# Performance work log

Measured on AMD Instinct MI355X. Metric: run time of the kernel, lower is better.

## Reference

```python
import jax, jax.numpy as jnp
import numpy as np
from jax import lax


def _kaiming_uniform(key, shape):
    fan_in = shape[1]
    bound = np.sqrt(6.0 / fan_in)
    return jax.random.uniform(key, shape, jnp.float32, -bound, bound)


def rbf_conv(x, w, k, pad):
    # x: [B,C,H,W]; w: [O, C*k*k]. Equivalent to F.unfold + torch.cdist (p=2).
    patches = lax.conv_general_dilated_patches(
        x, (k, k), (1, 1), [(pad, pad), (pad, pad)])  # [B, C*k*k, Ho, Wo]
    B, D, Ho, Wo = patches.shape
    p = patches.reshape(B, D, Ho * Wo)                 # [B, D, L]
    pn = jnp.sum(p * p, axis=1)                        # [B, L]
    wn = jnp.sum(w * w, axis=1)                        # [O]
    cross = jnp.einsum('bdl,od->bol', p, w)            # [B, O, L]
    d2 = pn[:, None, :] + wn[None, :, None] - 2.0 * cross
    d = jnp.sqrt(jnp.maximum(d2, 0.0))
    return d.reshape(B, w.shape[0], Ho, Wo)


def sfm(x, alpha):
    # non-overlapping (fh,fw) blocks, elementwise alpha weight, mean-pool
    B, C, H, W = x.shape
    fh, fw = alpha.shape
    xb = x.reshape(B, C, H // fh, fh, W // fw, fw).transpose(0, 1, 2, 4, 3, 5)
    return jnp.mean(xb * alpha, axis=(-2, -1))         # [B,C,H//fh,W//fw]


def gauss_act(d, std):
    return jnp.exp(d * d / (-2.0 * std * std))


def crelu(x, bias):
    return x * (x >= bias).astype(x.dtype)


def basic_block(x, w, std, bias, alpha, k, pad):
    d = rbf_conv(x, w, k, pad)
    return sfm(crelu(gauss_act(d, std), bias), alpha)


def setup_inputs() -> dict:
    key = jax.random.key(0)
    ks = jax.random.split(key, 8)
    x = jax.random.normal(ks[0], (16, 3, 128, 128), jnp.float32)
    w1 = _kaiming_uniform(ks[1], (96, 3 * 5 * 5))
    w2 = _kaiming_uniform(ks[2], (192, 96 * 5 * 5))
    w3 = _kaiming_uniform(ks[3], (384, 192 * 3 * 3))
    alpha = jnp.linspace(0.9, 0.99, 4, dtype=jnp.float32).reshape(2, 2)
    fc_w = jax.random.normal(ks[4], (100, 384 * 32 * 32), jnp.float32) * 0.01
    fc_b = jnp.zeros((100,), jnp.float32)
    return {
        'x': x,
        'w1': w1, 'std1': jnp.array([2.0], jnp.float32), 'bias1': jnp.array([0.3], jnp.float32), 'alpha1': alpha,
        'w2': w2, 'std2': jnp.array([2.0], jnp.float32), 'bias2': jnp.array([0.3], jnp.float32), 'alpha2': alpha,
        'w3': w3, 'std3': jnp.array([2.0], jnp.float32), 'bias3': jnp.array([0.3], jnp.float32),
        'fc_w': fc_w, 'fc_b': fc_b,
    }


def reference(x, w1, std1, bias1, alpha1, w2, std2, bias2, alpha2,
              w3, std3, bias3, fc_w, fc_b):
    h = basic_block(x, w1, std1, bias1, alpha1, 5, 2)      # [16,96,64,64]
    h = basic_block(h, w2, std2, bias2, alpha2, 5, 2)      # [16,192,32,32]
    d = rbf_conv(h, w3, 3, 1)                              # [16,384,32,32]
    h = crelu(gauss_act(d, std3), bias3)
    out = h.reshape(x.shape[0], -1) @ fc_w.T + fc_b        # [16,100]
    return out
```

## Files before the change

### kernel.cpp

```cpp
#include <hip/hip_runtime.h>

#define TPB 256

typedef short bf16x8 __attribute__((ext_vector_type(8)));
typedef float f32x4 __attribute__((ext_vector_type(4)));

__device__ inline unsigned short f2bf(float f) {
    unsigned int u = __float_as_uint(f);
    unsigned int r = (u + 0x7fffu + ((u >> 16) & 1u)) >> 16;
    return (unsigned short)r;
}
__device__ inline float bf2f(unsigned short h) {
    return __uint_as_float(((unsigned int)h) << 16);
}

__device__ __forceinline__ void gl16(void* lds, const void* g) {
    __builtin_amdgcn_global_load_lds(
        (const __attribute__((address_space(1))) unsigned int*)g,
        (__attribute__((address_space(3))) unsigned int*)lds, 16, 0, 0);
}

__global__ void prep_all(const float* __restrict__ x,
                         const float* __restrict__ w1, const float* __restrict__ w2,
                         const float* __restrict__ w3,
                         unsigned short* __restrict__ xbf,
                         unsigned short* __restrict__ w1r, unsigned short* __restrict__ w2r,
                         unsigned short* __restrict__ w3r, unsigned short* __restrict__ zerob,
                         float* __restrict__ wn1, float* __restrict__ wn2,
                         float* __restrict__ wn3) {
    int bid = blockIdx.x;
    int tid = threadIdx.x;
    if (bid < 1024) {
        int idx = bid * TPB + tid;
        int b = idx >> 14, px = idx & 16383;
        const float* xb = x + (size_t)b * 3 * 16384 + px;
        float v0 = xb[0], v1 = xb[16384], v2 = xb[32768];
        ushort4 v;
        v.x = f2bf(v0); v.y = f2bf(v1); v.z = f2bf(v2);
        v.w = f2bf(v0 * v0 + v1 * v1 + v2 * v2);
        *(ushort4*)&xbf[(size_t)idx * 4] = v;
    } else if (bid < 4388) {
        int idx = (bid - 1024) * TPB + tid;
        if (idx < 13056) {
            int o = idx / 136, d = idx - o * 136;
            int tp = d >> 2, c = d & 3;
            float v = 0.f;
            if (tp < 30) {
                int ki = tp / 6, kj = tp - 6 * ki;
                if (kj < 5) v = (c < 3) ? w1[o * 75 + c * 25 + ki * 5 + kj] : -0.5f;
            }
            w1r[idx] = f2bf(v);
        } else if (idx < 492288) {
            int i = idx - 13056;
            int c = i & 31; int r = i >> 5;
            int o = r % 192; r /= 192;
            int tap = r % 26; int cg = r / 26;
            float v = 0.f;
            if (tap < 25) v = w2[((size_t)o * 96 + cg * 32 + c) * 25 + tap];
            w2r[i] = f2bf(v);
        } else if (idx < 860928) {
            int i = idx - 492288;
            int c = i & 31; int r = i >> 5;
            int o = r % 192; r /= 192;
            int tap = r % 10; int cg = r / 10;
            float v = 0.f;
            if (tap < 9) v = w3[((size_t)o * 192 + cg * 32 + c) * 9 + tap];
            w3r[i] = f2bf(v);
        } else if (idx < 860992) {
            zerob[idx - 860928] = 0;
        }
    } else {
        int o = (bid - 4388) * 4 + (tid >> 6);
        int lane = tid & 63;
        const float* row; float* dst; int D;
        if (o < 96)       { row = w1 + (size_t)o * 75;           D = 75;   dst = wn1 + o; }
        else if (o < 288) { int r = o - 96;  row = w2 + (size_t)r * 2400; D = 2400; dst = wn2 + r; }
        else              { int r = o - 288; row = w3 + (size_t)r * 1728; D = 1728; dst = wn3 + r; }
        float acc = 0.f;
        for (int i = lane; i < D; i += 64) { float v = row[i]; acc += v * v; }
        #pragma unroll
        for (int off = 32; off >= 1; off >>= 1) acc += __shfl_down(acc, off);
        if (lane == 0) *dst = acc;
    }
}

__launch_bounds__(256, 2)
__global__ void conv1_mfma(const unsigned short* __restrict__ xbf,
                           const unsigned short* __restrict__ w1r,
                           const float* __restrict__ wn,
                           const float* __restrict__ stdp, const float* __restrict__ biasp,
                           const float* __restrict__ alphap,
                           unsigned short* __restrict__ out,
                           float* __restrict__ sqout)
{
    __shared__ unsigned short in_s[22 * 20 * 4];
    __shared__ unsigned short w_s[96 * 136];

    int bid = blockIdx.x;
    int tx = bid & 7; bid >>= 3;
    int ty = bid & 7; bid >>= 3;
    int b = bid;
    int x0 = tx * 16, y0 = ty * 16;
    int tid = threadIdx.x;
    int lane = tid & 63, wv = tid >> 6;
    int col = lane & 15, kg = lane >> 4;

    for (int idx = tid; idx < 21 * 20; idx += 256) {
        int py = idx / 20, px = idx - py * 20;
        int gy = y0 - 2 + py, gx = x0 - 2 + px;
        ushort4 v = make_ushort4(0, 0, 0, 0);
        if (gy >= 0 && gy < 128 && gx >= 0 && gx < 128)
            v = *(const ushort4*)&xbf[(((size_t)b * 128 + gy) * 128 + gx) * 4];
        *(ushort4*)&in_s[idx * 4] = v;
    }
    for (int idx = tid; idx < 1632; idx += 256)
        *(bf16x8*)&w_s[idx * 8] = *(const bf16x8*)&w1r[idx * 8];
    __syncthreads();

    f32x4 acc[6][4];
    #pragma unroll
    for (int mt = 0; mt < 6; ++mt)
        #pragma unroll
        for (int n = 0; n < 4; ++n) acc[mt][n] = (f32x4){0.f, 0.f, 0.f, 0.f};

    #pragma unroll
    for (int ks = 0; ks < 4; ++ks) {
        int tap0 = ks * 8 + kg * 2;
        int ki = tap0 / 6, kj = tap0 - 6 * ki;
        bf16x8 bfrag[4];
        #pragma unroll
        for (int n = 0; n < 4; ++n) {
            int row = wv * 4 + n + ki;
            int ix = col + kj;
            const unsigned short* p = &in_s[(row * 20 + ix) * 4];
            union { bf16x8 v; uint2 u[2]; } tmp;
            tmp.u[0] = *(const uint2*)p;
            tmp.u[1] = *(const uint2*)(p + 4);
            bfrag[n] = tmp.v;
        }
        bf16x8 afrag[6];
        #pragma unroll
        for (int mt = 0; mt < 6; ++mt)
            afrag[mt] = *(const bf16x8*)&w_s[(mt * 16 + col) * 136 + ks * 32 + kg * 8];
        #pragma unroll
        for (int mt = 0; mt < 6; ++mt)
            #pragma unroll
            for (int n = 0; n < 4; ++n)
                acc[mt][n] = __builtin_amdgcn_mfma_f32_16x16x32_bf16(
                    afrag[mt], bfrag[n], acc[mt][n], 0, 0, 0);
    }

    float stdv = stdp[0], biasv = biasp[0];
    float inv2s2 = 1.f / (2.f * stdv * stdv);
    float a00 = alphap[0], a01 = alphap[1], a10 = alphap[2], a11 = alphap[3];
    int dx = col & 1;
    float ax0 = dx ? a01 : a00;
    float ax1 = dx ? a11 : a10;

    float sqa[2] = {0.f, 0.f};
    #pragma unroll
    for (int mt = 0; mt < 6; ++mt) {
        #pragma unroll
        for (int p2 = 0; p2 < 2; ++p2) {
            unsigned short res[4];
            #pragma unroll
            for (int r = 0; r < 4; ++r) {
                int o = mt * 16 + kg * 4 + r;
                float wno = wn[o];
                float d20 = fmaxf(wno - 2.f * acc[mt][2 * p2][r], 0.f);
                float d21 = fmaxf(wno - 2.f * acc[mt][2 * p2 + 1][r], 0.f);
                float g0 = __expf(-d20 * inv2s2);
                float g1 = __expf(-d21 * inv2s2);
                g0 = (g0 >= biasv) ? g0 : 0.f;
                g1 = (g1 >= biasv) ? g1 : 0.f;
                float s = ax0 * g0 + ax1 * g1;
                s += __shfl_xor(s, 1);
                res[r] = f2bf(0.25f * s);
                float vv = bf2f(res[r]);
                sqa[p2] += vv * vv;
            }
            if (dx == 0) {
                int yo = ty * 8 + wv * 2 + p2, xo = tx * 8 + (col >> 1);
                *(ushort4*)&out[(((size_t)b * 64 + yo) * 64 + xo) * 96 + mt * 16 + kg * 4] =
                    make_ushort4(res[0], res[1], res[2], res[3]);
            }
        }
    }
    #pragma unroll
    for (int p2 = 0; p2 < 2; ++p2) {
        float s = sqa[p2];
        s += __shfl_xor(s, 16);
        s += __shfl_xor(s, 32);
        if (dx == 0 && kg == 0) {
            int yo = ty * 8 + wv * 2 + p2, xo = tx * 8 + (col >> 1);
            sqout[((size_t)b * 64 + yo) * 64 + xo] = s;
        }
    }
}

__launch_bounds__(128, 2)
__global__ void conv2_mfma(const unsigned short* __restrict__ hin,
                           const unsigned short* __restrict__ wt2,
                           const float* __restrict__ sq1,
                           const float* __restrict__ wn,
                           const float* __restrict__ stdp, const float* __restrict__ biasp,
                           const float* __restrict__ alphap,
                           const unsigned short* __restrict__ zerob,
                           unsigned short* __restrict__ hout)
{
    __shared__ unsigned short in_s[240 * 32];
    __shared__ unsigned short w_s[2][2 * 96 * 32];
    __shared__ float sq_s[12 * 20];
    __shared__ int s_nz[2];

    int bid = blockIdx.x;
    int xt = bid & 3; bid >>= 2;
    int yt = bid & 7; bid >>= 3;
    int ot = bid & 1; int b = bid >> 1;
    int x0 = xt * 16, y0 = yt * 8, o0 = ot * 96;
    int tid = threadIdx.x;
    int lane = tid & 63, wave_n = tid >> 6;
    int col = lane & 15, kg = lane >> 4;

    #pragma unroll
    for (int i = 0; i < 2; ++i) {
        int sidx = tid + i * 128;
        if (sidx < 240) {
            int r = sidx / 20, c = sidx - r * 20;
            int gy = y0 - 2 + r, gx = x0 - 2 + c;
            float v = 0.f;
            if (gy >= 0 && gy < 64 && gx >= 0 && gx < 64)
                v = sq1[((size_t)b * 64 + gy) * 64 + gx];
            sq_s[sidx] = v;
        }
    }

    f32x4 acc[6][4];
    #pragma unroll
    for (int mt = 0; mt < 6; ++mt)
        #pragma unroll
        for (int nt = 0; nt < 4; ++nt) acc[mt][nt] = (f32x4){0.f, 0.f, 0.f, 0.f};

    for (int cg = 0; cg < 3; ++cg) {
        #pragma unroll
        for (int i = 0; i < 8; ++i) {
            int chunk = tid + i * 128;
            if (chunk < 960) {
                int px = chunk >> 2, c16 = chunk & 3;
                int iy = px / 20, ix = px - iy * 20;
                int gy = y0 - 2 + iy, gx = x0 - 2 + ix;
                const void* src = (gy >= 0 && gy < 64 && gx >= 0 && gx < 64)
                    ? (const void*)&hin[(((size_t)b * 64 + gy) * 64 + gx) * 96 + cg * 32 + c16 * 8]
                    : (const void*)zerob;
                gl16(&in_s[chunk * 8], src);
            }
        }
        #pragma unroll
        for (int i = 0; i < 6; ++i) {
            int chunk = tid + i * 128;
            int tp = chunk / 384, rem = chunk - tp * 384;
            gl16(&w_s[0][tp * 3072 + rem * 8],
                 &wt2[(((size_t)cg * 26 + tp) * 192 + o0) * 32 + rem * 8]);
        }
        __syncthreads();

        unsigned int nzb = 0;
        #pragma unroll
        for (int i = 0; i < 8; ++i) {
            int chunk = tid + i * 128;
            if (chunk < 960) {
                uint4 v = *(const uint4*)&in_s[chunk * 8];
                nzb |= v.x | v.y | v.z | v.w;
            }
        }
        bool any = __any(nzb != 0);
        if (lane == 0) s_nz[wave_n] = any ? 1 : 0;
        __syncthreads();
        if (s_nz[0] | s_nz[1]) {
            for (int pr = 0; pr < 13; ++pr) {
                int cur = pr & 1;
                if (pr < 12) {
                    #pragma unroll
                    for (int i = 0; i < 6; ++i) {
                        int chunk = tid + i * 128;
                        int tp = chunk / 384, rem = chunk - tp * 384;
                        gl16(&w_s[cur ^ 1][tp * 3072 + rem * 8],
                             &wt2[(((size_t)cg * 26 + (pr + 1) * 2 + tp) * 192 + o0) * 32 + rem * 8]);
                    }
                }
                #pragma unroll
                for (int t2 = 0; t2 < 2; ++t2) {
                    int tap = pr * 2 + t2;
                    int ki = tap / 5, kj = tap - 5 * ki;
                    if (tap >= 25) { ki = 0; kj = 0; }
                    bf16x8 bfrag[4], afrag[6];
                    #pragma unroll
                    for (int nt = 0; nt < 4; ++nt) {
                        int yy = 2 * nt + (col >> 3) + ki;
                        int xx = wave_n * 8 + (col & 7) + kj;
                        bfrag[nt] = *(const bf16x8*)&in_s[(yy * 20 + xx) * 32 + kg * 8];
                    }
                    #pragma unroll
                    for (int mt = 0; mt < 6; ++mt)
                        afrag[mt] = *(const bf16x8*)
                            &w_s[cur][(t2 * 96 + mt * 16 + col) * 32 + kg * 8];
                    #pragma unroll
                    for (int mt = 0; mt < 6; ++mt)
                        #pragma unroll
                        for (int nt = 0; nt < 4; ++nt)
                            acc[mt][nt] = __builtin_amdgcn_mfma_f32_16x16x32_bf16(
                                afrag[mt], bfrag[nt], acc[mt][nt], 0, 0, 0);
                }
                __syncthreads();
            }
        }
    }

    float stdv = stdp[0], biasv = biasp[0];
    float inv2s2 = 1.f / (2.f * stdv * stdv);
    float a_own = alphap[(col >> 3) * 2 + (col & 1)];
    #pragma unroll
    for (int nt = 0; nt < 4; ++nt) {
        int ly = 2 * nt + (col >> 3) + 2;
        int lx = wave_n * 8 + (col & 7) + 2;
        float pnv = 0.f;
        #pragma unroll
        for (int dy = -2; dy <= 2; ++dy)
            #pragma unroll
            for (int dx2 = -2; dx2 <= 2; ++dx2)
                pnv += sq_s[(ly + dy) * 20 + (lx + dx2)];
        int y = y0 + 2 * nt + (col >> 3);
        int x = x0 + wave_n * 8 + (col & 7);
        int yo = (y0 >> 1) + nt;
        int xo = x >> 1;
        #pragma unroll
        for (int mt = 0; mt < 6; ++mt) {
            int ob = o0 + mt * 16 + (kg << 2);
            unsigned short res[4];
            #pragma unroll
            for (int r = 0; r < 4; ++r) {
                float d2 = fmaxf(pnv + wn[ob + r] - 2.f * acc[mt][nt][r], 0.f);
                float g = __expf(-d2 * inv2s2);
                g = (g >= biasv) ? g : 0.f;
                g *= a_own;
                g += __shfl_xor(g, 1);
                g += __shfl_xor(g, 8);
                res[r] = f2bf(0.25f * g);
            }
            if (((col & 1) == 0) && ((col & 8) == 0)) {
                *(ushort4*)&hout[(((size_t)b * 32 + yo) * 32 + xo) * 192 + ob] =
                    make_ushort4(res[0], res[1], res[2], res[3]);
            }
        }
        (void)y;
    }
}

__launch_bounds__(256, 1)
__global__ void conv3_mfma(const unsigned short* __restrict__ hin,
                           const unsigned short* __restrict__ wt3,
                           const float* __restrict__ wn,
                           const float* __restrict__ stdp, const float* __restrict__ biasp,
                           const unsigned short* __restrict__ zerob,
                           unsigned short* __restrict__ hout)
{
    __shared__ unsigned short in_s[324 * 32];
    __shared__ unsigned short w_s[2][2 * 96 * 32];
    __shared__ float pnacc[324];

    int bid = blockIdx.x;
    int sp = bid & 3; bid >>= 2;
    int ot = bid & 3; int b = bid >> 2;
    int x0 = (sp & 1) * 16, y0 = (sp >> 1) * 16, o0 = ot * 96;
    int tid = threadIdx.x;
    int lane = tid & 63, wvn = tid >> 6;
    int col = lane & 15, kg = lane >> 4;

    for (int i = tid; i < 324; i += 256) pnacc[i] = 0.f;

    f32x4 acc[6][4];
    #pragma unroll
    for (int mt = 0; mt < 6; ++mt)
        #pragma unroll
        for (int nt = 0; nt < 4; ++nt) acc[mt][nt] = (f32x4){0.f, 0.f, 0.f, 0.f};

    for (int cg = 0; cg < 6; ++cg) {
        #pragma unroll
        for (int i = 0; i < 6; ++i) {
            int chunk = tid + i * 256;
            if (chunk < 1296) {
                int px = chunk >> 2, c16 = chunk & 3;
                int iy = px / 18, ix = px - iy * 18;
                int gy = y0 - 1 + iy, gx = x0 - 1 + ix;
                const void* src = (gy >= 0 && gy < 32 && gx >= 0 && gx < 32)
                    ? (const void*)&hin[(((size_t)b * 32 + gy) * 32 + gx) * 192 + cg * 32 + c16 * 8]
                    : (const void*)zerob;
                gl16(&in_s[chunk * 8], src);
            }
        }
        #pragma unroll
        for (int i = 0; i < 3; ++i) {
            int chunk = tid + i * 256;
            int tp = chunk / 384, rem = chunk - tp * 384;
            gl16(&w_s[0][tp * 3072 + rem * 8],
                 &wt3[(((size_t)cg * 10 + tp) * 192 + o0) * 32 + rem * 8]);
        }
        __syncthreads();

        #pragma unroll
        for (int i = 0; i < 2; ++i) {
            int px = tid + i * 256;
            if (px < 324) {
                const unsigned short* p = &in_s[px * 32];
                float a = 0.f;
                #pragma unroll
                for (int c = 0; c < 32; c += 8) {
                    bf16x8 v = *(const bf16x8*)&p[c];
                    #pragma unroll
                    for (int j = 0; j < 8; ++j) { float f = bf2f((unsigned short)v[j]); a += f * f; }
                }
                pnacc[px] += a;
            }
        }

        for (int pr = 0; pr < 5; ++pr) {
            int cur = pr & 1;
            if (pr < 4) {
                #pragma unroll
                for (int i = 0; i < 3; ++i) {
                    int chunk = tid + i * 256;
                    int tp = chunk / 384, rem = chunk - tp * 384;
                    gl16(&w_s[cur ^ 1][tp * 3072 + rem * 8],
                         &wt3[(((size_t)cg * 10 + (pr + 1) * 2 + tp) * 192 + o0) * 32 + rem * 8]);
                }
            }
            #pragma unroll
            for (int t2 = 0; t2 < 2; ++t2) {
                int tap = pr * 2 + t2;
                int ki = tap / 3, kj = tap - 3 * ki;
                if (tap >= 9) { ki = 0; kj = 0; }
                bf16x8 bfrag[4], afrag[6];
                #pragma unroll
                for (int nt = 0; nt < 4; ++nt)
                    bfrag[nt] = *(const bf16x8*)
                        &in_s[((wvn * 4 + nt + ki) * 18 + col + kj) * 32 + kg * 8];
                #pragma unroll
                for (int mt = 0; mt < 6; ++mt)
                    afrag[mt] = *(const bf16x8*)
                        &w_s[cur][(t2 * 96 + mt * 16 + col) * 32 + kg * 8];
                #pragma unroll
                for (int mt = 0; mt < 6; ++mt)
                    #pragma unroll
                    for (int nt = 0; nt < 4; ++nt)
                        acc[mt][nt] = __builtin_amdgcn_mfma_f32_16x16x32_bf16(
                            afrag[mt], bfrag[nt], acc[mt][nt], 0, 0, 0);
            }
            __syncthreads();
        }
    }

    float stdv = stdp[0], biasv = biasp[0];
    float inv2s2 = 1.f / (2.f * stdv * stdv);
    #pragma unroll
    for (int nt = 0; nt < 4; ++nt) {
        int y = y0 + wvn * 4 + nt;
        int x = x0 + col;
        int ly = wvn * 4 + nt + 1, lx = col + 1;
        float pnv = 0.f;
        #pragma unroll
        for (int dy = -1; dy <= 1; ++dy)
            #pragma unroll
            for (int dx = -1; dx <= 1; ++dx)
                pnv += pnacc[(ly + dy) * 18 + (lx + dx)];
        #pragma unroll
        for (int mt = 0; mt < 6; ++mt) {
            int ob = o0 + mt * 16 + (kg << 2);
            #pragma unroll
            for (int r = 0; r < 4; ++r) {
                float d2 = fmaxf(pnv + wn[ob + r] - 2.f * acc[mt][nt][r], 0.f);
                float g = __expf(-d2 * inv2s2);
                g = (g >= biasv) ? g : 0.f;
                hout[((size_t)b * 384 + ob + r) * 1024 + y * 32 + x] = f2bf(g);
            }
        }
    }
}

__launch_bounds__(256, 4)
__global__ void fc_mfma(const unsigned short* __restrict__ h3bf,
                        const float* __restrict__ fw,
                        float* __restrict__ fcp,
                        int* __restrict__ flags)
{
    __shared__ unsigned short h3s[16 * 520];
    __shared__ unsigned short fws[16 * 520];
    __shared__ float red[4][16][16];
    __shared__ int s_nz[4];
    const size_t KI = 393216;
    int ch = blockIdx.x;
    int i0 = ch * 512;
    int tid = threadIdx.x;
    int lane = tid & 63, wv = tid >> 6;
    int col = lane & 15, kg = lane >> 4;

    unsigned int nzbits = 0;
    #pragma unroll
    for (int it = 0; it < 4; ++it) {
        int c = tid + it * 256;
        int b = c >> 6, off = (c & 63) * 8;
        bf16x8 v = *(const bf16x8*)&h3bf[(size_t)b * KI + i0 + off];
        union { bf16x8 s; unsigned int u[4]; } cv; cv.s = v;
        nzbits |= cv.u[0] | cv.u[1] | cv.u[2] | cv.u[3];
        *(bf16x8*)&h3s[b * 520 + off] = v;
    }
    bool any = __any(nzbits != 0);
    if (lane == 0) s_nz[wv] = any ? 1 : 0;
    __syncthreads();
    int anyall = s_nz[0] | s_nz[1] | s_nz[2] | s_nz[3];
    if (!anyall) {
        if (tid == 0) flags[ch] = 0;
        return;
    }
    if (tid == 0) flags[ch] = 1;

    float4 pre[8];
    #pragma unroll
    for (int it = 0; it < 8; ++it) {
        int c = tid + it * 256;
        int row = c >> 7, off4 = (c & 127) * 4;
        pre[it] = (row < 100) ? *(const float4*)&fw[(size_t)row * KI + i0 + off4]
                              : make_float4(0.f, 0.f, 0.f, 0.f);
    }

    for (int jt = 0; jt < 7; ++jt) {
        int j0 = jt * 16;
        #pragma unroll
        for (int it = 0; it < 8; ++it) {
            int c = tid + it * 256;
            int row = c >> 7, off4 = (c & 127) * 4;
            *(ushort4*)&fws[row * 520 + off4] =
                make_ushort4(f2bf(pre[it].x), f2bf(pre[it].y), f2bf(pre[it].z), f2bf(pre[it].w));
        }
        if (jt < 6) {
            #pragma unroll
            for (int it = 0; it < 8; ++it) {
                int c = tid + it * 256;
                int row = c >> 7, off4 = (c & 127) * 4;
                int j = j0 + 16 + row;
                pre[it] = (j < 100) ? *(const float4*)&fw[(size_t)j * KI + i0 + off4]
                                    : make_float4(0.f, 0.f, 0.f, 0.f);
            }
        }
        __syncthreads();
        f32x4 acc = (f32x4){0.f, 0.f, 0.f, 0.f};
        #pragma unroll
        for (int s = 0; s < 4; ++s) {
            int k = wv * 128 + s * 32 + kg * 8;
            bf16x8 af = *(const bf16x8*)&fws[col * 520 + k];
            bf16x8 bg = *(const bf16x8*)&h3s[col * 520 + k];
            acc = __builtin_amdgcn_mfma_f32_16x16x32_bf16(af, bg, acc, 0, 0, 0);
        }
        #pragma unroll
        for (int r = 0; r < 4; ++r) red[wv][kg * 4 + r][col] = acc[r];
        __syncthreads();
        int j = tid >> 4, bb = tid & 15;
        float s = red[0][j][bb] + red[1][j][bb] + red[2][j][bb] + red[3][j][bb];
        fcp[((size_t)ch * 112 + j0 + j) * 16 + bb] = s;
    }
}

__global__ void fc_final(const float* __restrict__ fcp, const int* __restrict__ flags,
                         const float* __restrict__ fb, float* __restrict__ outp) {
    int j = blockIdx.x;
    int lane = threadIdx.x;
    float acc[16];
    #pragma unroll
    for (int b = 0; b < 16; ++b) acc[b] = 0.f;
    for (int ch = lane; ch < 768; ch += 64) {
        if (flags[ch]) {
            const float* p = &fcp[((size_t)ch * 112 + j) * 16];
            #pragma unroll
            for (int b = 0; b < 16; ++b) acc[b] += p[b];
        }
    }
    #pragma unroll
    for (int off = 32; off >= 1; off >>= 1)
        #pragma unroll
        for (int b = 0; b < 16; ++b) acc[b] += __shfl_down(acc[b], off);
    if (lane == 0) {
        float bj = fb[j];
        #pragma unroll
        for (int b = 0; b < 16; ++b) outp[b * 100 + j] = bj + acc[b];
    }
}

extern "C" void kernel_launch(void* const* d_in, const int* in_sizes, int n_in,
                              void* d_out, int out_size, void* d_ws, size_t ws_size,
                              hipStream_t stream) {
    const float* x      = (const float*)d_in[0];
    const float* w1     = (const float*)d_in[1];
    const float* std1   = (const float*)d_in[2];
    const float* bias1  = (const float*)d_in[3];
    const float* alpha1 = (const float*)d_in[4];
    const float* w2     = (const float*)d_in[5];
    const float* std2   = (const float*)d_in[6];
    const float* bias2  = (const float*)d_in[7];
    const float* alpha2 = (const float*)d_in[8];
    const float* w3     = (const float*)d_in[9];
    const float* std3   = (const float*)d_in[10];
    const float* bias3  = (const float*)d_in[11];
    const float* fc_w   = (const float*)d_in[12];
    const float* fc_b   = (const float*)d_in[13];
    float* out = (float*)d_out;
    float* ws  = (float*)d_ws;

    float* sbuf  = ws;
    float* fcp   = sbuf + 65536;
    float* wn1   = fcp + 1376256;
    float* wn2   = wn1 + 96;
    float* wn3   = wn2 + 192;
    int*   flags = (int*)(wn3 + 384);
    float* rest  = wn3 + 384 + 768 + 32;
    unsigned short* h1bf = (unsigned short*)rest;
    unsigned short* h2bf = h1bf + 6291456;
    unsigned short* h3bf = h2bf + 3145728;
    unsigned short* xbf  = h3bf + 6291456;
    unsigned short* w1r  = xbf + 1048576;
    unsigned short* w2r  = w1r + 13056;
    unsigned short* w3r  = w2r + 479232;
    unsigned short* zerob = w3r + 368640;

    dim3 B(TPB);

    prep_all<<<dim3(4556), B, 0, stream>>>(x, w1, w2, w3, xbf, w1r, w2r, w3r, zerob,
                                           wn1, wn2, wn3);

    conv1_mfma<<<dim3(1024), B, 0, stream>>>(xbf, w1r, wn1, std1, bias1, alpha1,
                                             h1bf, sbuf);

    conv2_mfma<<<dim3(1024), dim3(128), 0, stream>>>(
        h1bf, w2r, sbuf, wn2, std2, bias2, alpha2, zerob, h2bf);

    conv3_mfma<<<dim3(256), B, 0, stream>>>(
        h2bf, w3r, wn3, std3, bias3, zerob, h3bf);

    fc_mfma<<<dim3(768), B, 0, stream>>>(h3bf, fc_w, fcp, flags);
    fc_final<<<dim3(100), dim3(64), 0, stream>>>(fcp, flags, fc_b, out);
}
```

Baseline: 107.6 us.

## Split conv3 into smaller spatial tiles and defer conv2 weight prefetch past zero check

conv3 now uses 16x8 spatial tiles with 512 blocks instead of 256. Each wave covers 48 output channels and 32 pixels (3x4 MFMA tiles instead of 6x4), and launch bounds allow 2 blocks per CU. This is meant to fill the GPU's compute units better and cut accumulator register pressure, at the cost of more halo reloads of input rows. Separately, conv2 now issues its first weight-tile prefetch only after the all-zero input check, so skipped channel groups no longer load weights, at the cost of an extra barrier.

```diff
diff --git a/kernel.cpp b/kernel.cpp
--- a/kernel.cpp
+++ b/kernel.cpp
@@ -255,13 +255,6 @@
                 gl16(&in_s[chunk * 8], src);
             }
         }
-        #pragma unroll
-        for (int i = 0; i < 6; ++i) {
-            int chunk = tid + i * 128;
-            int tp = chunk / 384, rem = chunk - tp * 384;
-            gl16(&w_s[0][tp * 3072 + rem * 8],
-                 &wt2[(((size_t)cg * 26 + tp) * 192 + o0) * 32 + rem * 8]);
-        }
         __syncthreads();
 
         unsigned int nzb = 0;
@@ -277,6 +270,14 @@
         if (lane == 0) s_nz[wave_n] = any ? 1 : 0;
         __syncthreads();
         if (s_nz[0] | s_nz[1]) {
+            #pragma unroll
+            for (int i = 0; i < 6; ++i) {
+                int chunk = tid + i * 128;
+                int tp = chunk / 384, rem = chunk - tp * 384;
+                gl16(&w_s[0][tp * 3072 + rem * 8],
+                     &wt2[(((size_t)cg * 26 + tp) * 192 + o0) * 32 + rem * 8]);
+            }
+            __syncthreads();
             for (int pr = 0; pr < 13; ++pr) {
                 int cur = pr & 1;
                 if (pr < 12) {
@@ -329,7 +330,6 @@
             #pragma unroll
             for (int dx2 = -2; dx2 <= 2; ++dx2)
                 pnv += sq_s[(ly + dy) * 20 + (lx + dx2)];
-        int y = y0 + 2 * nt + (col >> 3);
         int x = x0 + wave_n * 8 + (col & 7);
         int yo = (y0 >> 1) + nt;
         int xo = x >> 1;
@@ -352,11 +352,10 @@
                     make_ushort4(res[0], res[1], res[2], res[3]);
             }
         }
-        (void)y;
-    }
-}
-
-__launch_bounds__(256, 1)
+    }
+}
+
+__launch_bounds__(256, 2)
 __global__ void conv3_mfma(const unsigned short* __restrict__ hin,
                            const unsigned short* __restrict__ wt3,
                            const float* __restrict__ wn,
@@ -364,31 +363,33 @@
                            const unsigned short* __restrict__ zerob,
                            unsigned short* __restrict__ hout)
 {
-    __shared__ unsigned short in_s[324 * 32];
+    __shared__ unsigned short in_s[180 * 32];
     __shared__ unsigned short w_s[2][2 * 96 * 32];
-    __shared__ float pnacc[324];
+    __shared__ float pnacc[180];
 
     int bid = blockIdx.x;
-    int sp = bid & 3; bid >>= 2;
+    int sp = bid & 7; bid >>= 3;
     int ot = bid & 3; int b = bid >> 2;
-    int x0 = (sp & 1) * 16, y0 = (sp >> 1) * 16, o0 = ot * 96;
+    int x0 = (sp & 1) * 16, y0 = (sp >> 1) * 8, o0 = ot * 96;
     int tid = threadIdx.x;
-    int lane = tid & 63, wvn = tid >> 6;
+    int lane = tid & 63, wid = tid >> 6;
+    int om = wid >> 1, wn2 = wid & 1;
     int col = lane & 15, kg = lane >> 4;
-
-    for (int i = tid; i < 324; i += 256) pnacc[i] = 0.f;
-
-    f32x4 acc[6][4];
-    #pragma unroll
-    for (int mt = 0; mt < 6; ++mt)
+    int coly = col >> 3, colx = col & 7;
+
+    if (tid < 180) pnacc[tid] = 0.f;
+
+    f32x4 acc[3][4];
+    #pragma unroll
+    for (int mt = 0; mt < 3; ++mt)
         #pragma unroll
         for (int nt = 0; nt < 4; ++nt) acc[mt][nt] = (f32x4){0.f, 0.f, 0.f, 0.f};
 
     for (int cg = 0; cg < 6; ++cg) {
         #pragma unroll
-        for (int i = 0; i < 6; ++i) {
+        for (int i = 0; i < 3; ++i) {
             int chunk = tid + i * 256;
-            if (chunk < 1296) {
+            if (chunk < 720) {
                 int px = chunk >> 2, c16 = chunk & 3;
                 int iy = px / 18, ix = px - iy * 18;
                 int gy = y0 - 1 + iy, gx = x0 - 1 + ix;
@@ -407,20 +408,16 @@
         }
         __syncthreads();
 
-        #pragma unroll
-        for (int i = 0; i < 2; ++i) {
-            int px = tid + i * 256;
-            if (px < 324) {
-                const unsigned short* p = &in_s[px * 32];
-                float a = 0.f;
+        if (tid < 180) {
+            const unsigned short* p = &in_s[tid * 32];
+            float a = 0.f;
+            #pragma unroll
+            for (int c = 0; c < 32; c += 8) {
+                bf16x8 v = *(const bf16x8*)&p[c];
                 #pragma unroll
-                for (int c = 0; c < 32; c += 8) {
-                    bf16x8 v = *(const bf16x8*)&p[c];
-                    #pragma unroll
-                    for (int j = 0; j < 8; ++j) { float f = bf2f((unsigned short)v[j]); a += f * f; }
-                }
-                pnacc[px] += a;
-            }
+                for (int j = 0; j < 8; ++j) { float f = bf2f((unsigned short)v[j]); a += f * f; }
+            }
+            pnacc[tid] += a;
         }
 
         for (int pr = 0; pr < 5; ++pr) {
@@ -439,17 +436,19 @@
                 int tap = pr * 2 + t2;
                 int ki = tap / 3, kj = tap - 3 * ki;
                 if (tap >= 9) { ki = 0; kj = 0; }
-                bf16x8 bfrag[4], afrag[6];
+                bf16x8 bfrag[4], afrag[3];
                 #pragma unroll
-                for (int nt = 0; nt < 4; ++nt)
-                    bfrag[nt] = *(const bf16x8*)
-                        &in_s[((wvn * 4 + nt + ki) * 18 + col + kj) * 32 + kg * 8];
+                for (int nt = 0; nt < 4; ++nt) {
+                    int yy = 2 * nt + coly + ki;
+                    int xx = wn2 * 8 + colx + kj;
+                    bfrag[nt] = *(const bf16x8*)&in_s[(yy * 18 + xx) * 32 + kg * 8];
+                }
                 #pragma unroll
-                for (int mt = 0; mt < 6; ++mt)
+                for (int mt = 0; mt < 3; ++mt)
                     afrag[mt] = *(const bf16x8*)
-                        &w_s[cur][(t2 * 96 + mt * 16 + col) * 32 + kg * 8];
+                        &w_s[cur][(t2 * 96 + om * 48 + mt * 16 + col) * 32 + kg * 8];
                 #pragma unroll
-                for (int mt = 0; mt < 6; ++mt)
+                for (int mt = 0; mt < 3; ++mt)
                     #pragma unroll
                     for (int nt = 0; nt < 4; ++nt)
                         acc[mt][nt] = __builtin_amdgcn_mfma_f32_16x16x32_bf16(
@@ -463,9 +462,9 @@
     float inv2s2 = 1.f / (2.f * stdv * stdv);
     #pragma unroll
     for (int nt = 0; nt < 4; ++nt) {
-        int y = y0 + wvn * 4 + nt;
-        int x = x0 + col;
-        int ly = wvn * 4 + nt + 1, lx = col + 1;
+        int y = y0 + 2 * nt + coly;
+        int x = x0 + wn2 * 8 + colx;
+        int ly = 2 * nt + coly + 1, lx = wn2 * 8 + colx + 1;
         float pnv = 0.f;
         #pragma unroll
         for (int dy = -1; dy <= 1; ++dy)
@@ -473,8 +472,8 @@
             for (int dx = -1; dx <= 1; ++dx)
                 pnv += pnacc[(ly + dy) * 18 + (lx + dx)];
         #pragma unroll
-        for (int mt = 0; mt < 6; ++mt) {
-            int ob = o0 + mt * 16 + (kg << 2);
+        for (int mt = 0; mt < 3; ++mt) {
+            int ob = o0 + om * 48 + mt * 16 + (kg << 2);
             #pragma unroll
             for (int r = 0; r < 4; ++r) {
                 float d2 = fmaxf(pnv + wn[ob + r] - 2.f * acc[mt][nt][r], 0.f);
@@ -641,7 +640,7 @@
     conv2_mfma<<<dim3(1024), dim3(128), 0, stream>>>(
         h1bf, w2r, sbuf, wn2, std2, bias2, alpha2, zerob, h2bf);
 
-    conv3_mfma<<<dim3(256), B, 0, stream>>>(
+    conv3_mfma<<<dim3(512), B, 0, stream>>>(
         h2bf, w3r, wn3, std3, bias3, zerob, h3bf);
 
     fc_mfma<<<dim3(768), B, 0, stream>>>(h3bf, fc_w, fcp, flags);
```

After: 102.4 us. 4.9% less time.
